# Optimization experiments

Hardware: AMD Instinct MI355X
Metric: run time of the kernel (lower is better)

The kernel has to match this reference:

```python
import jax, jax.numpy as jnp
import numpy as np

NT = 100000   # total word nodes (B graphs * N nodes)
B = 50        # number of graphs in the batch
E = 1600000   # total edges
V = 15000     # vocab (num_word)
D_IN = 128    # h_inp
D_H = 128     # h_dim


def setup_inputs() -> dict:
    key = jax.random.key(0)
    ks = jax.random.split(key, 12)
    return {
        "node_ids": jax.random.randint(ks[0], (NT,), 0, V),
        "src": jax.random.randint(ks[1], (E,), 0, NT),
        "dst": jax.random.randint(ks[2], (E,), 0, NT),
        "edge_weight": jax.random.uniform(ks[3], (E,), dtype=jnp.float32),
        "y_data": jax.random.uniform(ks[4], (B,), dtype=jnp.float32),
        "word_embeds": jax.random.normal(ks[5], (V, D_IN), dtype=jnp.float32) * 0.1,
        "W1": jax.random.normal(ks[6], (D_IN, D_H), dtype=jnp.float32) * 0.05,
        "b1": jax.random.normal(ks[7], (D_H,), dtype=jnp.float32) * 0.05,
        "W2": jax.random.normal(ks[8], (D_H, D_H), dtype=jnp.float32) * 0.05,
        "b2": jax.random.normal(ks[9], (D_H,), dtype=jnp.float32) * 0.05,
        "W_out": jax.random.normal(ks[10], (D_H, 1), dtype=jnp.float32) * 0.05,
        "b_out": jax.random.normal(ks[11], (1,), dtype=jnp.float32) * 0.05,
    }


def _word_graph_layer(h, W, b, src, dst, edge_weight, deg):
    # Linear projection, then DGL u_mul_e + mean aggregation over incoming edges.
    Wh = h @ W + b                                   # [NT, D]
    m = Wh[src] * edge_weight[:, None]               # gather + edge-weight mul, [E, D]
    s = jax.ops.segment_sum(m, dst, num_segments=NT)  # scatter-add, [NT, D]
    # mean over incoming messages; nodes with no in-edges keep 0 (DGL semantics)
    return jnp.where(deg[:, None] > 0, s / jnp.maximum(deg, 1.0)[:, None], 0.0)


def reference(node_ids, src, dst, edge_weight, y_data, word_embeds,
              W1, b1, W2, b2, W_out, b_out):
    deg = jax.ops.segment_sum(jnp.ones_like(edge_weight), dst, num_segments=NT)
    h = word_embeds[node_ids]                        # [NT, D_IN]
    h = _word_graph_layer(h, W1, b1, src, dst, edge_weight, deg)
    h = jax.nn.leaky_relu(h, negative_slope=0.01)
    h = _word_graph_layer(h, W2, b2, src, dst, edge_weight, deg)
    # per-graph mean pool; equal graph sizes so padded mean == true mean
    word_pool = h.reshape(B, NT // B, D_H).mean(axis=1)   # [B, D_H]
    logits = (word_pool @ W_out + b_out).reshape(-1)      # [B]
    # binary_cross_entropy_with_logits, mean reduction (numerically stable)
    loss = jnp.mean(jnp.maximum(logits, 0.0) - logits * y_data
                    + jnp.log1p(jnp.exp(-jnp.abs(logits))))
    y_pred = jax.nn.sigmoid(logits)[:, None]              # [B, 1]
    return (loss, y_pred)
```

## Files before the change

### kernel.cpp

```cpp
#include <hip/hip_runtime.h>
#include <hip/hip_fp16.h>
#include <math.h>

#define NT 100000
#define B_GRAPHS 50
#define NE 1600000
#define V 15000
#define D 128
#define NODES_PER_GRAPH (NT / B_GRAPHS)

#define POOL_N (B_GRAPHS * D + B_GRAPHS)

#define BSH 8
#define BIN_DSTS 256
#define NBIN ((NT + BIN_DSTS - 1) / BIN_DSTS)
#define SLACK (3 * BIN_DSTS)
#define EPB 4096
#define NFB ((NE + EPB - 1) / EPB)
#define BUF_SORT 5632
#define STAGE_STRIDE 4608
#define PAY_STRIDE (STAGE_STRIDE + SLACK)
#define PAY_TAIL 512

__device__ __forceinline__ unsigned enc2_e5m2(float a, float b) {
  unsigned ha = __half_as_ushort(__float2half(a));
  unsigned hb = __half_as_ushort(__float2half(b));
  ha = ((ha + 0x7fu + ((ha >> 8) & 1u)) >> 8) & 0xffu;
  hb = ((hb + 0x7fu + ((hb >> 8) & 1u)) >> 8) & 0xffu;
  return ha | (hb << 8);
}
__device__ __forceinline__ unsigned enc4_e5m2(float a, float b, float c, float d) {
  return enc2_e5m2(a, b) | (enc2_e5m2(c, d) << 16);
}

#define PR 16
__global__ __launch_bounds__(256, 8)
void k_project(const float* __restrict__ embeds,
               const float* __restrict__ W1,
               const float* __restrict__ b1,
               unsigned* __restrict__ P1p8,
               int* __restrict__ binCursor, float* __restrict__ pool,
               int2* __restrict__ payTail) {
  __shared__ float sE[PR][D];
  __shared__ float sO[PR][D];
  int t = threadIdx.x;
  if (blockIdx.x == 0) {
    for (int i = t; i < 512; i += 256) binCursor[i] = 0;
    for (int i = t; i < POOL_N; i += 256) pool[i] = 0.f;
    for (int i = t; i < PAY_TAIL; i += 256) payTail[i] = make_int2(0, 0);
  }
  int row0 = blockIdx.x * PR;
  for (int i = t; i < PR * D; i += 256) {
    int r = i >> 7, c = i & 127;
    int v = row0 + r;
    sE[r][c] = (v < V) ? embeds[(size_t)v * D + c] : 0.f;
  }
  __syncthreads();
  int c = t & 127, rg = (t >> 7) * 8;
  float bd = b1[c];
  float acc[8];
#pragma unroll
  for (int r = 0; r < 8; ++r) acc[r] = bd;
#pragma unroll 4
  for (int k = 0; k < D; ++k) {
    float w = W1[k * D + c];
#pragma unroll
    for (int r = 0; r < 8; ++r) acc[r] = fmaf(sE[rg + r][k], w, acc[r]);
  }
#pragma unroll
  for (int r = 0; r < 8; ++r) sO[rg + r][c] = acc[r];
  __syncthreads();
  for (int i = t; i < PR * 32; i += 256) {
    int r = i >> 5, li = i & 31;
    int v = row0 + r;
    if (v < V)
      P1p8[(size_t)v * 32 + li] =
          enc4_e5m2(sO[r][4 * li], sO[r][4 * li + 1], sO[r][4 * li + 2], sO[r][4 * li + 3]);
  }
}

__global__ __launch_bounds__(512)
void k_binfill(const int* __restrict__ src, const int* __restrict__ dst,
               const float* __restrict__ ew, const int* __restrict__ node_ids,
               int* __restrict__ binCursor, int2* __restrict__ stage) {
  __shared__ int h[512], sc[512], gbase[512], cur[512];
  __shared__ int wsum[8], woff[8];
  __shared__ unsigned short binOf[EPB];
  __shared__ int2 buf[EPB];
  int t = threadIdx.x;
  int lane = t & 63, wv = t >> 6;
  h[t] = 0;
  __syncthreads();
  int base = blockIdx.x * EPB;
  int d_[EPB / 512], b_[EPB / 512];
#pragma unroll
  for (int i = 0; i < EPB / 512; ++i) {
    int e = base + i * 512 + t;
    int d = (e < NE) ? dst[e] : -1;
    d_[i] = d;
    b_[i] = (d >= 0) ? (d >> BSH) : -1;
    if (d >= 0) atomicAdd(&h[b_[i]], 1);
  }
  __syncthreads();
  int c = h[t];
  int v = c;
#pragma unroll
  for (int off = 1; off < 64; off <<= 1) {
    int x = __shfl_up(v, off);
    if (lane >= off) v += x;
  }
  if (lane == 63) wsum[wv] = v;
  __syncthreads();
  if (t == 0) {
    int a = 0;
#pragma unroll
    for (int i = 0; i < 8; ++i) { woff[i] = a; a += wsum[i]; }
  }
  __syncthreads();
  int incl = v + woff[wv];
  sc[t] = incl;
  cur[t] = incl - c;
  if (t < NBIN && c > 0) gbase[t] = atomicAdd(&binCursor[t], c);
  __syncthreads();
  int total = sc[511];
#pragma unroll
  for (int i = 0; i < EPB / 512; ++i) {
    int e = base + i * 512 + t;
    if (e < NE) {
      int s = src[e];
      unsigned uw = __float_as_uint(ew[e]);
      unsigned wb = (uw + 0x7fffu + ((uw >> 16) & 1u)) & 0xffff0000u;
      int wid = node_ids[s];
      int dl = d_[i] & (BIN_DSTS - 1);
      int p = atomicAdd(&cur[b_[i]], 1);
      buf[p] = make_int2((int)(wb | (unsigned)wid), s | (dl << 17));
      binOf[p] = (unsigned short)b_[i];
    }
  }
  __syncthreads();
  for (int i = t; i < total; i += 512) {
    int b = binOf[i];
    int local = i - (sc[b] - h[b]);
    stage[(size_t)b * STAGE_STRIDE + gbase[b] + local] = buf[i];
  }
}

__global__ __launch_bounds__(512)
void k_binsort(const int2* __restrict__ stage, const int* __restrict__ binCnt,
               int* __restrict__ rowD, int* __restrict__ cntD,
               int2* __restrict__ pay) {
  __shared__ int h2[BIN_DSTS], cur2[BIN_DSTS];
  __shared__ float invD[BIN_DSTS];
  __shared__ int wsum4[4], woff4[4];
  __shared__ int sh_end;
  __shared__ int2 buf[BUF_SORT];
  int b = blockIdx.x, t = threadIdx.x;
  int lane = t & 63, wv = t >> 6;
  int cnt = binCnt[b];
  int sb = b * STAGE_STRIDE;
  int pb = b * PAY_STRIDE;
  int dst0 = b << BSH;
  if (t < BIN_DSTS) h2[t] = 0;
  __syncthreads();
  for (int i = t; i < cnt; i += 512)
    atomicAdd(&h2[(stage[sb + i].y >> 17) & 255], 1);
  __syncthreads();
  int c = (t < BIN_DSTS) ? h2[t] : 0;
  int pc = (c + 3) & ~3;
  int v = (t < BIN_DSTS) ? pc : 0;
#pragma unroll
  for (int off = 1; off < 64; off <<= 1) {
    int x = __shfl_up(v, off);
    if (lane >= off) v += x;
  }
  if (lane == 63 && wv < 4) wsum4[wv] = v;
  __syncthreads();
  if (t == 0) {
    int a = 0;
#pragma unroll
    for (int i = 0; i < 4; ++i) { woff4[i] = a; a += wsum4[i]; }
    sh_end = a;
  }
  __syncthreads();
  if (t < BIN_DSTS) {
    int myoff = v + woff4[wv] - pc;
    invD[t] = (c > 0) ? (1.0f / (float)c) : 0.0f;
    cur2[t] = myoff;
    int n = dst0 + t;
    if (n < NT) { rowD[n] = pb + myoff; cntD[n] = c; }
  }
  __syncthreads();
  int end = sh_end + 24;
  if (end > PAY_STRIDE) end = PAY_STRIDE;
  for (int i = t; i < end; i += 512) buf[i] = make_int2(0, 0);
  __syncthreads();
  for (int i = t; i < cnt; i += 512) {
    int2 r = stage[sb + i];
    int dl = (r.y >> 17) & 255;
    float w = __uint_as_float((unsigned)r.x & 0xffff0000u);
    float wp = w * invD[dl];
    unsigned wh = (unsigned)__half_as_ushort(__float2half(wp));
    int p = atomicAdd(&cur2[dl], 1);
    buf[p] = make_int2((int)((wh << 16) | ((unsigned)r.x & 0xffffu)), r.y & 0x1ffff);
  }
  __syncthreads();
  for (int i = t; i < end; i += 512) pay[pb + i] = buf[i];
}

template<bool USE_WID>
__device__ __forceinline__ int pick_idx(const int4& q, int half) {
  int lo = USE_WID ? (q.x & 0xffff) : q.y;
  int hi = USE_WID ? (q.z & 0xffff) : q.w;
  return half ? hi : lo;
}
__device__ __forceinline__ void consume2h(const int4& q, unsigned v, int half,
                                          __half2& A01, __half2& A23, __half2& SW) {
  unsigned wm = (unsigned)(half ? q.z : q.x);
  unsigned wd = (wm >> 16) | (wm & 0xffff0000u);
  unsigned hp0 = ((v & 0xffu) << 8) | ((v & 0xff00u) << 16);
  unsigned hp1 = ((v >> 8) & 0xff00u) | (v & 0xff000000u);
  __half2 w2 = *(__half2*)&wd;
  A01 = __hfma2(w2, *(__half2*)&hp0, A01);
  A23 = __hfma2(w2, *(__half2*)&hp1, A23);
  SW = __hadd2(SW, w2);
}

template<bool USE_WID>
__device__ __forceinline__ void gather_row(const int2* __restrict__ pay,
                                           const unsigned* __restrict__ tab,
                                           int beg, int cnt, int li, int half,
                                           __half2& A01, __half2& A23, __half2& SW) {
  int G = (cnt + 3) >> 2;
  const int4* __restrict__ pp = (const int4*)(pay + beg);
  int4 q0a = pp[0], q0b = pp[1];
  int4 q1a = pp[2], q1b = pp[3];
  int4 q2a = pp[4], q2b = pp[5];
  int4 q3a = pp[6], q3b = pp[7];
  int4 q4a = pp[8], q4b = pp[9];
  unsigned va0 = tab[(size_t)pick_idx<USE_WID>(q0a, half) * 32 + li];
  unsigned vb0 = tab[(size_t)pick_idx<USE_WID>(q0b, half) * 32 + li];
  unsigned va1 = tab[(size_t)pick_idx<USE_WID>(q1a, half) * 32 + li];
  unsigned vb1 = tab[(size_t)pick_idx<USE_WID>(q1b, half) * 32 + li];
  unsigned va2 = tab[(size_t)pick_idx<USE_WID>(q2a, half) * 32 + li];
  unsigned vb2 = tab[(size_t)pick_idx<USE_WID>(q2b, half) * 32 + li];
  for (int g = 0; g < G; ++g) {
    unsigned vn0 = tab[(size_t)pick_idx<USE_WID>(q3a, half) * 32 + li];
    unsigned vn1 = tab[(size_t)pick_idx<USE_WID>(q3b, half) * 32 + li];
    int4 qna = pp[2 * g + 10];
    int4 qnb = pp[2 * g + 11];
    consume2h(q0a, va0, half, A01, A23, SW);
    consume2h(q0b, vb0, half, A01, A23, SW);
    q0a = q1a; q0b = q1b; q1a = q2a; q1b = q2b; q2a = q3a; q2b = q3b;
    q3a = q4a; q3b = q4b; q4a = qna; q4b = qnb;
    va0 = va1; vb0 = vb1; va1 = va2; vb1 = vb2; va2 = vn0; vb2 = vn1;
  }
}

#define NPW1 10
__global__ void k_agg1(const int2* __restrict__ pay,
                       const int* __restrict__ rowD, const int* __restrict__ cntD,
                       const unsigned* __restrict__ P1p8,
                       unsigned* __restrict__ h1p8) {
  int w = threadIdx.x >> 6, lane = threadIdx.x & 63;
  int li = lane & 31, half = lane >> 5;
  int nbase = blockIdx.x * (4 * NPW1) + w * NPW1;
  for (int i = 0; i < NPW1; ++i) {
    int n = nbase + i;
    int beg = __builtin_amdgcn_readfirstlane(rowD[n]);
    int cnt = __builtin_amdgcn_readfirstlane(cntD[n]);
    __half2 A01 = __half2half2(__float2half(0.f));
    __half2 A23 = A01, SW = A01;
    gather_row<true>(pay, P1p8, beg, cnt, li, half, A01, A23, SW);
    float2 f01 = __half22float2(A01);
    float2 f23 = __half22float2(A23);
    float a0 = f01.x, a1 = f01.y, a2 = f23.x, a3 = f23.y;
    a0 += __shfl_down(a0, 32);
    a1 += __shfl_down(a1, 32);
    a2 += __shfl_down(a2, 32);
    a3 += __shfl_down(a3, 32);
    if (lane < 32) {
      float x0 = a0, x1 = a1, x2 = a2, x3 = a3;
      x0 = (x0 > 0.f) ? x0 : 0.01f * x0;
      x1 = (x1 > 0.f) ? x1 : 0.01f * x1;
      x2 = (x2 > 0.f) ? x2 : 0.01f * x2;
      x3 = (x3 > 0.f) ? x3 : 0.01f * x3;
      h1p8[(size_t)n * 32 + li] = enc4_e5m2(x0, x1, x2, x3);
    }
  }
}

#define NPW2 10
#define BLKS_PER_G (NODES_PER_GRAPH / (4 * NPW2))
__global__ void k_agg2(const int2* __restrict__ pay,
                       const int* __restrict__ rowD, const int* __restrict__ cntD,
                       const unsigned* __restrict__ h1p8,
                       float* __restrict__ pool) {
  int g = blockIdx.x / BLKS_PER_G;
  int chunk = blockIdx.x % BLKS_PER_G;
  int w = threadIdx.x >> 6, lane = threadIdx.x & 63;
  int li = lane & 31, half = lane >> 5;
  int nbase = g * NODES_PER_GRAPH + chunk * (4 * NPW2) + w * NPW2;
  __half2 A01 = __half2half2(__float2half(0.f));
  __half2 A23 = A01, SW = A01;
  for (int i = 0; i < NPW2; ++i) {
    int n = nbase + i;
    int beg = __builtin_amdgcn_readfirstlane(rowD[n]);
    int cnt = __builtin_amdgcn_readfirstlane(cntD[n]);
    gather_row<false>(pay, h1p8, beg, cnt, li, half, A01, A23, SW);
  }
  float2 f01 = __half22float2(A01);
  float2 f23 = __half22float2(A23);
  float s0 = f01.x, s1 = f01.y, s2 = f23.x, s3 = f23.y;
  float sc = __low2float(SW);
  s0 += __shfl_down(s0, 32);
  s1 += __shfl_down(s1, 32);
  s2 += __shfl_down(s2, 32);
  s3 += __shfl_down(s3, 32);
  sc += __shfl_down(sc, 32);
  __shared__ float sS[4 * 128];
  __shared__ float sC[4];
  if (lane < 32) {
    sS[w * 128 + 4 * li + 0] = s0;
    sS[w * 128 + 4 * li + 1] = s1;
    sS[w * 128 + 4 * li + 2] = s2;
    sS[w * 128 + 4 * li + 3] = s3;
  }
  if (lane == 0) sC[w] = sc;
  __syncthreads();
  int t = threadIdx.x;
  if (t < 128) {
    float v = sS[t] + sS[128 + t] + sS[256 + t] + sS[384 + t];
    atomicAdd(&pool[g * D + t], v);
  }
  if (t == 0) atomicAdd(&pool[B_GRAPHS * D + g], sC[0] + sC[1] + sC[2] + sC[3]);
}

__global__ void k_final(const float* __restrict__ poolS, const float* __restrict__ poolC,
                        const float* __restrict__ W2, const float* __restrict__ b2,
                        const float* __restrict__ W_out, const float* __restrict__ b_out,
                        const float* __restrict__ y, float* __restrict__ out) {
  __shared__ float w2o[D];
  __shared__ float s2oArr[D];
  __shared__ float s2o_sh;
  __shared__ float logits[64];
  int t = threadIdx.x;
  int w = t >> 6, lane = t & 63;
  if (t < D) {
    float acc = 0.f;
    for (int d = 0; d < D; ++d) acc = fmaf(W2[t * D + d], W_out[d], acc);
    w2o[t] = acc;
  } else {
    int j = t - D;
    s2oArr[j] = b2[j] * W_out[j];
  }
  __syncthreads();
  if (t < 64) {
    float v = s2oArr[lane] + s2oArr[64 + lane];
#pragma unroll
    for (int off = 32; off > 0; off >>= 1) v += __shfl_down(v, off);
    if (lane == 0) s2o_sh = v;
  }
  __syncthreads();
  float s2o = s2o_sh;
  float bout = b_out[0];
  const float invN = 1.0f / (float)NODES_PER_GRAPH;
  for (int g = w; g < B_GRAPHS; g += 4) {
    float v = poolS[g * D + lane] * w2o[lane]
            + poolS[g * D + 64 + lane] * w2o[64 + lane];
#pragma unroll
    for (int off = 32; off > 0; off >>= 1) v += __shfl_down(v, off);
    if (lane == 0) {
      float l = v * invN + poolC[g] * invN * s2o + bout;
      logits[g] = l;
      out[1 + g] = 1.0f / (1.0f + expf(-l));
    }
  }
  __syncthreads();
  if (t < 64) {
    float term = 0.f;
    if (lane < B_GRAPHS) {
      float l = logits[lane];
      term = fmaxf(l, 0.f) - l * y[lane] + log1pf(expf(-fabsf(l)));
    }
#pragma unroll
    for (int off = 32; off > 0; off >>= 1) term += __shfl_down(term, off);
    if (lane == 0) out[0] = term / (float)B_GRAPHS;
  }
}

extern "C" void kernel_launch(void* const* d_in, const int* in_sizes, int n_in,
                              void* d_out, int out_size, void* d_ws, size_t ws_size,
                              hipStream_t stream) {
  const int*   node_ids = (const int*)d_in[0];
  const int*   src      = (const int*)d_in[1];
  const int*   dst      = (const int*)d_in[2];
  const float* ew       = (const float*)d_in[3];
  const float* y        = (const float*)d_in[4];
  const float* embeds   = (const float*)d_in[5];
  const float* W1       = (const float*)d_in[6];
  const float* b1       = (const float*)d_in[7];
  const float* W2       = (const float*)d_in[8];
  const float* b2       = (const float*)d_in[9];
  const float* W_out    = (const float*)d_in[10];
  const float* b_out    = (const float*)d_in[11];
  float* out = (float*)d_out;
  (void)in_sizes; (void)n_in; (void)out_size; (void)ws_size;

  char* ws = (char*)d_ws;
  size_t off = 0;
  auto alloc = [&](size_t bytes) {
    size_t r = off;
    off = (off + bytes + 511) & ~(size_t)511;
    return r;
  };
  size_t o_binCur = alloc(512 * 4);
  size_t o_pool   = alloc((size_t)POOL_N * 4);
  size_t o_rowD   = alloc((size_t)(NT + 1) * 4);
  size_t o_cntD   = alloc((size_t)NT * 4);
  size_t o_P1p8   = alloc((size_t)V * 32 * 4);
  size_t o_h1p8   = alloc((size_t)NT * 32 * 4);
  size_t o_stage  = alloc((size_t)NBIN * STAGE_STRIDE * 8);
  size_t o_pay    = alloc(((size_t)NBIN * PAY_STRIDE + PAY_TAIL) * 8);

  int*      binCursor= (int*)(ws + o_binCur);
  float*    pool     = (float*)(ws + o_pool);
  int*      rowD     = (int*)(ws + o_rowD);
  int*      cntD     = (int*)(ws + o_cntD);
  unsigned* P1p8     = (unsigned*)(ws + o_P1p8);
  unsigned* h1p8     = (unsigned*)(ws + o_h1p8);
  int2*     stage    = (int2*)(ws + o_stage);
  int2*     pay      = (int2*)(ws + o_pay);
  int2*     payTail  = pay + (size_t)NBIN * PAY_STRIDE;

  k_project<<<(V + PR - 1) / PR, 256, 0, stream>>>(embeds, W1, b1, P1p8,
                                                   binCursor, pool, payTail);
  k_binfill<<<NFB, 512, 0, stream>>>(src, dst, ew, node_ids, binCursor, stage);
  k_binsort<<<NBIN, 512, 0, stream>>>(stage, binCursor, rowD, cntD, pay);
  k_agg1<<<NT / (4 * NPW1), 256, 0, stream>>>(pay, rowD, cntD, P1p8, h1p8);
  k_agg2<<<B_GRAPHS * BLKS_PER_G, 256, 0, stream>>>(pay, rowD, cntD, h1p8, pool);
  k_final<<<1, 256, 0, stream>>>(pool, pool + B_GRAPHS * D, W2, b2, W_out, b_out, y, out);
}
```

Measured before the change: 253.7 us.

## Fuse projection with bin-fill and layer-1 aggregation into bin-sort kernel

```diff
diff --git a/kernel.cpp b/kernel.cpp
--- a/kernel.cpp
+++ b/kernel.cpp
@@ -21,6 +21,8 @@
 #define STAGE_STRIDE 4608
 #define PAY_STRIDE (STAGE_STRIDE + SLACK)
 #define PAY_TAIL 512
+#define PR 16
+#define PROJ_BLOCKS ((V + PR - 1) / PR)
 
 __device__ __forceinline__ unsigned enc2_e5m2(float a, float b) {
   unsigned ha = __half_as_ushort(__float2half(a));
@@ -31,180 +33,6 @@
 }
 __device__ __forceinline__ unsigned enc4_e5m2(float a, float b, float c, float d) {
   return enc2_e5m2(a, b) | (enc2_e5m2(c, d) << 16);
-}
-
-#define PR 16
-__global__ __launch_bounds__(256, 8)
-void k_project(const float* __restrict__ embeds,
-               const float* __restrict__ W1,
-               const float* __restrict__ b1,
-               unsigned* __restrict__ P1p8,
-               int* __restrict__ binCursor, float* __restrict__ pool,
-               int2* __restrict__ payTail) {
-  __shared__ float sE[PR][D];
-  __shared__ float sO[PR][D];
-  int t = threadIdx.x;
-  if (blockIdx.x == 0) {
-    for (int i = t; i < 512; i += 256) binCursor[i] = 0;
-    for (int i = t; i < POOL_N; i += 256) pool[i] = 0.f;
-    for (int i = t; i < PAY_TAIL; i += 256) payTail[i] = make_int2(0, 0);
-  }
-  int row0 = blockIdx.x * PR;
-  for (int i = t; i < PR * D; i += 256) {
-    int r = i >> 7, c = i & 127;
-    int v = row0 + r;
-    sE[r][c] = (v < V) ? embeds[(size_t)v * D + c] : 0.f;
-  }
-  __syncthreads();
-  int c = t & 127, rg = (t >> 7) * 8;
-  float bd = b1[c];
-  float acc[8];
-#pragma unroll
-  for (int r = 0; r < 8; ++r) acc[r] = bd;
-#pragma unroll 4
-  for (int k = 0; k < D; ++k) {
-    float w = W1[k * D + c];
-#pragma unroll
-    for (int r = 0; r < 8; ++r) acc[r] = fmaf(sE[rg + r][k], w, acc[r]);
-  }
-#pragma unroll
-  for (int r = 0; r < 8; ++r) sO[rg + r][c] = acc[r];
-  __syncthreads();
-  for (int i = t; i < PR * 32; i += 256) {
-    int r = i >> 5, li = i & 31;
-    int v = row0 + r;
-    if (v < V)
-      P1p8[(size_t)v * 32 + li] =
-          enc4_e5m2(sO[r][4 * li], sO[r][4 * li + 1], sO[r][4 * li + 2], sO[r][4 * li + 3]);
-  }
-}
-
-__global__ __launch_bounds__(512)
-void k_binfill(const int* __restrict__ src, const int* __restrict__ dst,
-               const float* __restrict__ ew, const int* __restrict__ node_ids,
-               int* __restrict__ binCursor, int2* __restrict__ stage) {
-  __shared__ int h[512], sc[512], gbase[512], cur[512];
-  __shared__ int wsum[8], woff[8];
-  __shared__ unsigned short binOf[EPB];
-  __shared__ int2 buf[EPB];
-  int t = threadIdx.x;
-  int lane = t & 63, wv = t >> 6;
-  h[t] = 0;
-  __syncthreads();
-  int base = blockIdx.x * EPB;
-  int d_[EPB / 512], b_[EPB / 512];
-#pragma unroll
-  for (int i = 0; i < EPB / 512; ++i) {
-    int e = base + i * 512 + t;
-    int d = (e < NE) ? dst[e] : -1;
-    d_[i] = d;
-    b_[i] = (d >= 0) ? (d >> BSH) : -1;
-    if (d >= 0) atomicAdd(&h[b_[i]], 1);
-  }
-  __syncthreads();
-  int c = h[t];
-  int v = c;
-#pragma unroll
-  for (int off = 1; off < 64; off <<= 1) {
-    int x = __shfl_up(v, off);
-    if (lane >= off) v += x;
-  }
-  if (lane == 63) wsum[wv] = v;
-  __syncthreads();
-  if (t == 0) {
-    int a = 0;
-#pragma unroll
-    for (int i = 0; i < 8; ++i) { woff[i] = a; a += wsum[i]; }
-  }
-  __syncthreads();
-  int incl = v + woff[wv];
-  sc[t] = incl;
-  cur[t] = incl - c;
-  if (t < NBIN && c > 0) gbase[t] = atomicAdd(&binCursor[t], c);
-  __syncthreads();
-  int total = sc[511];
-#pragma unroll
-  for (int i = 0; i < EPB / 512; ++i) {
-    int e = base + i * 512 + t;
-    if (e < NE) {
-      int s = src[e];
-      unsigned uw = __float_as_uint(ew[e]);
-      unsigned wb = (uw + 0x7fffu + ((uw >> 16) & 1u)) & 0xffff0000u;
-      int wid = node_ids[s];
-      int dl = d_[i] & (BIN_DSTS - 1);
-      int p = atomicAdd(&cur[b_[i]], 1);
-      buf[p] = make_int2((int)(wb | (unsigned)wid), s | (dl << 17));
-      binOf[p] = (unsigned short)b_[i];
-    }
-  }
-  __syncthreads();
-  for (int i = t; i < total; i += 512) {
-    int b = binOf[i];
-    int local = i - (sc[b] - h[b]);
-    stage[(size_t)b * STAGE_STRIDE + gbase[b] + local] = buf[i];
-  }
-}
-
-__global__ __launch_bounds__(512)
-void k_binsort(const int2* __restrict__ stage, const int* __restrict__ binCnt,
-               int* __restrict__ rowD, int* __restrict__ cntD,
-               int2* __restrict__ pay) {
-  __shared__ int h2[BIN_DSTS], cur2[BIN_DSTS];
-  __shared__ float invD[BIN_DSTS];
-  __shared__ int wsum4[4], woff4[4];
-  __shared__ int sh_end;
-  __shared__ int2 buf[BUF_SORT];
-  int b = blockIdx.x, t = threadIdx.x;
-  int lane = t & 63, wv = t >> 6;
-  int cnt = binCnt[b];
-  int sb = b * STAGE_STRIDE;
-  int pb = b * PAY_STRIDE;
-  int dst0 = b << BSH;
-  if (t < BIN_DSTS) h2[t] = 0;
-  __syncthreads();
-  for (int i = t; i < cnt; i += 512)
-    atomicAdd(&h2[(stage[sb + i].y >> 17) & 255], 1);
-  __syncthreads();
-  int c = (t < BIN_DSTS) ? h2[t] : 0;
-  int pc = (c + 3) & ~3;
-  int v = (t < BIN_DSTS) ? pc : 0;
-#pragma unroll
-  for (int off = 1; off < 64; off <<= 1) {
-    int x = __shfl_up(v, off);
-    if (lane >= off) v += x;
-  }
-  if (lane == 63 && wv < 4) wsum4[wv] = v;
-  __syncthreads();
-  if (t == 0) {
-    int a = 0;
-#pragma unroll
-    for (int i = 0; i < 4; ++i) { woff4[i] = a; a += wsum4[i]; }
-    sh_end = a;
-  }
-  __syncthreads();
-  if (t < BIN_DSTS) {
-    int myoff = v + woff4[wv] - pc;
-    invD[t] = (c > 0) ? (1.0f / (float)c) : 0.0f;
-    cur2[t] = myoff;
-    int n = dst0 + t;
-    if (n < NT) { rowD[n] = pb + myoff; cntD[n] = c; }
-  }
-  __syncthreads();
-  int end = sh_end + 24;
-  if (end > PAY_STRIDE) end = PAY_STRIDE;
-  for (int i = t; i < end; i += 512) buf[i] = make_int2(0, 0);
-  __syncthreads();
-  for (int i = t; i < cnt; i += 512) {
-    int2 r = stage[sb + i];
-    int dl = (r.y >> 17) & 255;
-    float w = __uint_as_float((unsigned)r.x & 0xffff0000u);
-    float wp = w * invD[dl];
-    unsigned wh = (unsigned)__half_as_ushort(__float2half(wp));
-    int p = atomicAdd(&cur2[dl], 1);
-    buf[p] = make_int2((int)((wh << 16) | ((unsigned)r.x & 0xffffu)), r.y & 0x1ffff);
-  }
-  __syncthreads();
-  for (int i = t; i < end; i += 512) pay[pb + i] = buf[i];
 }
 
 template<bool USE_WID>
@@ -224,53 +52,221 @@
   A23 = __hfma2(w2, *(__half2*)&hp1, A23);
   SW = __hadd2(SW, w2);
 }
-
-template<bool USE_WID>
-__device__ __forceinline__ void gather_row(const int2* __restrict__ pay,
-                                           const unsigned* __restrict__ tab,
-                                           int beg, int cnt, int li, int half,
-                                           __half2& A01, __half2& A23, __half2& SW) {
-  int G = (cnt + 3) >> 2;
-  const int4* __restrict__ pp = (const int4*)(pay + beg);
-  int4 q0a = pp[0], q0b = pp[1];
-  int4 q1a = pp[2], q1b = pp[3];
-  int4 q2a = pp[4], q2b = pp[5];
-  int4 q3a = pp[6], q3b = pp[7];
-  int4 q4a = pp[8], q4b = pp[9];
-  unsigned va0 = tab[(size_t)pick_idx<USE_WID>(q0a, half) * 32 + li];
-  unsigned vb0 = tab[(size_t)pick_idx<USE_WID>(q0b, half) * 32 + li];
-  unsigned va1 = tab[(size_t)pick_idx<USE_WID>(q1a, half) * 32 + li];
-  unsigned vb1 = tab[(size_t)pick_idx<USE_WID>(q1b, half) * 32 + li];
-  unsigned va2 = tab[(size_t)pick_idx<USE_WID>(q2a, half) * 32 + li];
-  unsigned vb2 = tab[(size_t)pick_idx<USE_WID>(q2b, half) * 32 + li];
-  for (int g = 0; g < G; ++g) {
-    unsigned vn0 = tab[(size_t)pick_idx<USE_WID>(q3a, half) * 32 + li];
-    unsigned vn1 = tab[(size_t)pick_idx<USE_WID>(q3b, half) * 32 + li];
-    int4 qna = pp[2 * g + 10];
-    int4 qnb = pp[2 * g + 11];
-    consume2h(q0a, va0, half, A01, A23, SW);
-    consume2h(q0b, vb0, half, A01, A23, SW);
-    q0a = q1a; q0b = q1b; q1a = q2a; q1b = q2b; q2a = q3a; q2b = q3b;
-    q3a = q4a; q3b = q4b; q4a = qna; q4b = qnb;
-    va0 = va1; vb0 = vb1; va1 = va2; vb1 = vb2; va2 = vn0; vb2 = vn1;
-  }
-}
-
-#define NPW1 10
-__global__ void k_agg1(const int2* __restrict__ pay,
-                       const int* __restrict__ rowD, const int* __restrict__ cntD,
-                       const unsigned* __restrict__ P1p8,
-                       unsigned* __restrict__ h1p8) {
-  int w = threadIdx.x >> 6, lane = threadIdx.x & 63;
+__device__ __forceinline__ void consume2h_ns(const int4& q, unsigned v, int half,
+                                             __half2& A01, __half2& A23) {
+  unsigned wm = (unsigned)(half ? q.z : q.x);
+  unsigned wd = (wm >> 16) | (wm & 0xffff0000u);
+  unsigned hp0 = ((v & 0xffu) << 8) | ((v & 0xff00u) << 16);
+  unsigned hp1 = ((v >> 8) & 0xff00u) | (v & 0xff000000u);
+  __half2 w2 = *(__half2*)&wd;
+  A01 = __hfma2(w2, *(__half2*)&hp0, A01);
+  A23 = __hfma2(w2, *(__half2*)&hp1, A23);
+}
+__device__ __forceinline__ int4 ld2s(const int2* bp, int i) {
+  int2 a = bp[i], c = bp[i + 1];
+  return make_int4(a.x, a.y, c.x, c.y);
+}
+
+__global__ __launch_bounds__(512)
+void k_pb(const float* __restrict__ embeds, const float* __restrict__ W1,
+          const float* __restrict__ b1, unsigned* __restrict__ P1p8,
+          float* __restrict__ pool, int2* __restrict__ payTail,
+          const int* __restrict__ src, const int* __restrict__ dst,
+          const float* __restrict__ ew, const int* __restrict__ node_ids,
+          int* __restrict__ binCursor, int2* __restrict__ stage) {
+  __shared__ union {
+    struct {
+      int h[512], sc[512], gbase[512], cur[512];
+      int wsum[8], woff[8];
+      unsigned short binOf[EPB];
+      int2 buf[EPB];
+    } f;
+    struct {
+      float sE[PR][D];
+      float sO[PR][D];
+    } p;
+  } U;
+  int t = threadIdx.x;
+  if (blockIdx.x < NFB) {
+    int lane = t & 63, wv = t >> 6;
+    U.f.h[t] = 0;
+    __syncthreads();
+    int base = blockIdx.x * EPB;
+    int d_[EPB / 512], b_[EPB / 512];
+#pragma unroll
+    for (int i = 0; i < EPB / 512; ++i) {
+      int e = base + i * 512 + t;
+      int d = (e < NE) ? dst[e] : -1;
+      d_[i] = d;
+      b_[i] = (d >= 0) ? (d >> BSH) : -1;
+      if (d >= 0) atomicAdd(&U.f.h[b_[i]], 1);
+    }
+    __syncthreads();
+    int c = U.f.h[t];
+    int v = c;
+#pragma unroll
+    for (int off = 1; off < 64; off <<= 1) {
+      int x = __shfl_up(v, off);
+      if (lane >= off) v += x;
+    }
+    if (lane == 63) U.f.wsum[wv] = v;
+    __syncthreads();
+    if (t == 0) {
+      int a = 0;
+#pragma unroll
+      for (int i = 0; i < 8; ++i) { U.f.woff[i] = a; a += U.f.wsum[i]; }
+    }
+    __syncthreads();
+    int incl = v + U.f.woff[wv];
+    U.f.sc[t] = incl;
+    U.f.cur[t] = incl - c;
+    if (t < NBIN && c > 0) U.f.gbase[t] = atomicAdd(&binCursor[t], c);
+    __syncthreads();
+    int total = U.f.sc[511];
+#pragma unroll
+    for (int i = 0; i < EPB / 512; ++i) {
+      int e = base + i * 512 + t;
+      if (e < NE) {
+        int s = src[e];
+        unsigned uw = __float_as_uint(ew[e]);
+        unsigned wb = (uw + 0x7fffu + ((uw >> 16) & 1u)) & 0xffff0000u;
+        int wid = node_ids[s];
+        int dl = d_[i] & (BIN_DSTS - 1);
+        int p = atomicAdd(&U.f.cur[b_[i]], 1);
+        U.f.buf[p] = make_int2((int)(wb | (unsigned)wid), s | (dl << 17));
+        U.f.binOf[p] = (unsigned short)b_[i];
+      }
+    }
+    __syncthreads();
+    for (int i = t; i < total; i += 512) {
+      int b = U.f.binOf[i];
+      int local = i - (U.f.sc[b] - U.f.h[b]);
+      stage[(size_t)b * STAGE_STRIDE + U.f.gbase[b] + local] = U.f.buf[i];
+    }
+  } else {
+    int pb = blockIdx.x - NFB;
+    if (pb == 0) {
+      for (int i = t; i < POOL_N; i += 512) pool[i] = 0.f;
+      for (int i = t; i < PAY_TAIL; i += 512) payTail[i] = make_int2(0, 0);
+    }
+    int row0 = pb * PR;
+    for (int i = t; i < PR * D; i += 512) {
+      int r = i >> 7, c = i & 127;
+      int vv = row0 + r;
+      U.p.sE[r][c] = (vv < V) ? embeds[(size_t)vv * D + c] : 0.f;
+    }
+    __syncthreads();
+    int c = t & 127, rg = (t >> 7) * 4;
+    float bd = b1[c];
+    float acc[4];
+#pragma unroll
+    for (int r = 0; r < 4; ++r) acc[r] = bd;
+#pragma unroll 4
+    for (int k = 0; k < D; ++k) {
+      float w = W1[k * D + c];
+#pragma unroll
+      for (int r = 0; r < 4; ++r) acc[r] = fmaf(U.p.sE[rg + r][k], w, acc[r]);
+    }
+#pragma unroll
+    for (int r = 0; r < 4; ++r) U.p.sO[rg + r][c] = acc[r];
+    __syncthreads();
+    {
+      int r = t >> 5, li = t & 31;
+      int vv = row0 + r;
+      if (vv < V)
+        P1p8[(size_t)vv * 32 + li] =
+            enc4_e5m2(U.p.sO[r][4 * li], U.p.sO[r][4 * li + 1],
+                      U.p.sO[r][4 * li + 2], U.p.sO[r][4 * li + 3]);
+    }
+  }
+}
+
+__global__ __launch_bounds__(512)
+void k_sortagg(const int2* __restrict__ stage, const int* __restrict__ binCnt,
+               const unsigned* __restrict__ P1p8,
+               int* __restrict__ rowD, int* __restrict__ cntD,
+               int2* __restrict__ pay, unsigned* __restrict__ h1p8) {
+  __shared__ int h2[BIN_DSTS], cur2[BIN_DSTS], offArr[BIN_DSTS];
+  __shared__ float invD[BIN_DSTS];
+  __shared__ int wsum4[4], woff4[4];
+  __shared__ int sh_end;
+  __shared__ int2 buf[BUF_SORT];
+  int b = blockIdx.x, t = threadIdx.x;
+  int lane = t & 63, wv = t >> 6;
+  int cnt = binCnt[b];
+  int sb = b * STAGE_STRIDE;
+  int pbase = b * PAY_STRIDE;
+  int dst0 = b << BSH;
+  if (t < BIN_DSTS) h2[t] = 0;
+  __syncthreads();
+  for (int i = t; i < cnt; i += 512)
+    atomicAdd(&h2[(stage[sb + i].y >> 17) & 255], 1);
+  __syncthreads();
+  int c = (t < BIN_DSTS) ? h2[t] : 0;
+  int pc = (c + 3) & ~3;
+  int v = (t < BIN_DSTS) ? pc : 0;
+#pragma unroll
+  for (int off = 1; off < 64; off <<= 1) {
+    int x = __shfl_up(v, off);
+    if (lane >= off) v += x;
+  }
+  if (lane == 63 && wv < 4) wsum4[wv] = v;
+  __syncthreads();
+  if (t == 0) {
+    int a = 0;
+#pragma unroll
+    for (int i = 0; i < 4; ++i) { woff4[i] = a; a += wsum4[i]; }
+    sh_end = a;
+  }
+  __syncthreads();
+  if (t < BIN_DSTS) {
+    int myoff = v + woff4[wv] - pc;
+    invD[t] = (c > 0) ? (1.0f / (float)c) : 0.0f;
+    cur2[t] = myoff;
+    offArr[t] = myoff;
+    int n = dst0 + t;
+    if (n < NT) { rowD[n] = pbase + myoff; cntD[n] = c; }
+  }
+  __syncthreads();
+  int end = sh_end + 24;
+  if (end > PAY_STRIDE) end = PAY_STRIDE;
+  for (int i = t; i < end; i += 512) buf[i] = make_int2(0, 0);
+  __syncthreads();
+  for (int i = t; i < cnt; i += 512) {
+    int2 r = stage[sb + i];
+    int dl = (r.y >> 17) & 255;
+    float w = __uint_as_float((unsigned)r.x & 0xffff0000u);
+    float wp = w * invD[dl];
+    unsigned wh = (unsigned)__half_as_ushort(__float2half(wp));
+    int p = atomicAdd(&cur2[dl], 1);
+    buf[p] = make_int2((int)((wh << 16) | ((unsigned)r.x & 0xffffu)), r.y & 0x1ffff);
+  }
+  __syncthreads();
+  for (int i = t; i < end; i += 512) pay[pbase + i] = buf[i];
   int li = lane & 31, half = lane >> 5;
-  int nbase = blockIdx.x * (4 * NPW1) + w * NPW1;
-  for (int i = 0; i < NPW1; ++i) {
-    int n = nbase + i;
-    int beg = __builtin_amdgcn_readfirstlane(rowD[n]);
-    int cnt = __builtin_amdgcn_readfirstlane(cntD[n]);
+  for (int j = 0; j < 32; ++j) {
+    int dl = wv * 32 + j;
+    int beg = offArr[dl];
+    int cn = h2[dl];
+    int G = (cn + 3) >> 2;
     __half2 A01 = __half2half2(__float2half(0.f));
-    __half2 A23 = A01, SW = A01;
-    gather_row<true>(pay, P1p8, beg, cnt, li, half, A01, A23, SW);
+    __half2 A23 = A01;
+    int4 qa0 = ld2s(buf, beg + 0), qb0 = ld2s(buf, beg + 2);
+    int4 qa1 = ld2s(buf, beg + 4), qb1 = ld2s(buf, beg + 6);
+    unsigned va0 = P1p8[(size_t)pick_idx<true>(qa0, half) * 32 + li];
+    unsigned vb0 = P1p8[(size_t)pick_idx<true>(qb0, half) * 32 + li];
+    unsigned va1 = P1p8[(size_t)pick_idx<true>(qa1, half) * 32 + li];
+    unsigned vb1 = P1p8[(size_t)pick_idx<true>(qb1, half) * 32 + li];
+    for (int g = 0; g < G; ++g) {
+      int4 qa2 = ld2s(buf, beg + 4 * g + 8);
+      int4 qb2 = ld2s(buf, beg + 4 * g + 10);
+      unsigned vn0 = P1p8[(size_t)pick_idx<true>(qa2, half) * 32 + li];
+      unsigned vn1 = P1p8[(size_t)pick_idx<true>(qb2, half) * 32 + li];
+      consume2h_ns(qa0, va0, half, A01, A23);
+      consume2h_ns(qb0, vb0, half, A01, A23);
+      qa0 = qa1; qb0 = qb1; qa1 = qa2; qb1 = qb2;
+      va0 = va1; vb0 = vb1; va1 = vn0; vb1 = vn1;
+    }
     float2 f01 = __half22float2(A01);
     float2 f23 = __half22float2(A23);
     float a0 = f01.x, a1 = f01.y, a2 = f23.x, a3 = f23.y;
@@ -279,13 +275,46 @@
     a2 += __shfl_down(a2, 32);
     a3 += __shfl_down(a3, 32);
     if (lane < 32) {
-      float x0 = a0, x1 = a1, x2 = a2, x3 = a3;
-      x0 = (x0 > 0.f) ? x0 : 0.01f * x0;
-      x1 = (x1 > 0.f) ? x1 : 0.01f * x1;
-      x2 = (x2 > 0.f) ? x2 : 0.01f * x2;
-      x3 = (x3 > 0.f) ? x3 : 0.01f * x3;
-      h1p8[(size_t)n * 32 + li] = enc4_e5m2(x0, x1, x2, x3);
-    }
+      int n = dst0 + dl;
+      if (n < NT) {
+        float x0 = a0, x1 = a1, x2 = a2, x3 = a3;
+        x0 = (x0 > 0.f) ? x0 : 0.01f * x0;
+        x1 = (x1 > 0.f) ? x1 : 0.01f * x1;
+        x2 = (x2 > 0.f) ? x2 : 0.01f * x2;
+        x3 = (x3 > 0.f) ? x3 : 0.01f * x3;
+        h1p8[(size_t)n * 32 + li] = enc4_e5m2(x0, x1, x2, x3);
+      }
+    }
+  }
+}
+
+__device__ __forceinline__ void gather_row_g(const int2* __restrict__ pay,
+                                             const unsigned* __restrict__ tab,
+                                             int beg, int cnt, int li, int half,
+                                             __half2& A01, __half2& A23, __half2& SW) {
+  int G = (cnt + 3) >> 2;
+  const int4* __restrict__ pp = (const int4*)(pay + beg);
+  int4 q0a = pp[0], q0b = pp[1];
+  int4 q1a = pp[2], q1b = pp[3];
+  int4 q2a = pp[4], q2b = pp[5];
+  int4 q3a = pp[6], q3b = pp[7];
+  int4 q4a = pp[8], q4b = pp[9];
+  unsigned va0 = tab[(size_t)pick_idx<false>(q0a, half) * 32 + li];
+  unsigned vb0 = tab[(size_t)pick_idx<false>(q0b, half) * 32 + li];
+  unsigned va1 = tab[(size_t)pick_idx<false>(q1a, half) * 32 + li];
+  unsigned vb1 = tab[(size_t)pick_idx<false>(q1b, half) * 32 + li];
+  unsigned va2 = tab[(size_t)pick_idx<false>(q2a, half) * 32 + li];
+  unsigned vb2 = tab[(size_t)pick_idx<false>(q2b, half) * 32 + li];
+  for (int g = 0; g < G; ++g) {
+    unsigned vn0 = tab[(size_t)pick_idx<false>(q3a, half) * 32 + li];
+    unsigned vn1 = tab[(size_t)pick_idx<false>(q3b, half) * 32 + li];
+    int4 qna = pp[2 * g + 10];
+    int4 qnb = pp[2 * g + 11];
+    consume2h(q0a, va0, half, A01, A23, SW);
+    consume2h(q0b, vb0, half, A01, A23, SW);
+    q0a = q1a; q0b = q1b; q1a = q2a; q1b = q2b; q2a = q3a; q2b = q3b;
+    q3a = q4a; q3b = q4b; q4a = qna; q4b = qnb;
+    va0 = va1; vb0 = vb1; va1 = va2; vb1 = vb2; va2 = vn0; vb2 = vn1;
   }
 }
 
@@ -306,7 +335,7 @@
     int n = nbase + i;
     int beg = __builtin_amdgcn_readfirstlane(rowD[n]);
     int cnt = __builtin_amdgcn_readfirstlane(cntD[n]);
-    gather_row<false>(pay, h1p8, beg, cnt, li, half, A01, A23, SW);
+    gather_row_g(pay, h1p8, beg, cnt, li, half, A01, A23, SW);
   }
   float2 f01 = __half22float2(A01);
   float2 f23 = __half22float2(A23);
@@ -432,11 +461,10 @@
   int2*     pay      = (int2*)(ws + o_pay);
   int2*     payTail  = pay + (size_t)NBIN * PAY_STRIDE;
 
-  k_project<<<(V + PR - 1) / PR, 256, 0, stream>>>(embeds, W1, b1, P1p8,
-                                                   binCursor, pool, payTail);
-  k_binfill<<<NFB, 512, 0, stream>>>(src, dst, ew, node_ids, binCursor, stage);
-  k_binsort<<<NBIN, 512, 0, stream>>>(stage, binCursor, rowD, cntD, pay);
-  k_agg1<<<NT / (4 * NPW1), 256, 0, stream>>>(pay, rowD, cntD, P1p8, h1p8);
+  hipMemsetAsync(binCursor, 0, 512 * 4, stream);
+  k_pb<<<NFB + PROJ_BLOCKS, 512, 0, stream>>>(embeds, W1, b1, P1p8, pool, payTail,
+                                              src, dst, ew, node_ids, binCursor, stage);
+  k_sortagg<<<NBIN, 512, 0, stream>>>(stage, binCursor, P1p8, rowD, cntD, pay, h1p8);
   k_agg2<<<B_GRAPHS * BLKS_PER_G, 256, 0, stream>>>(pay, rowD, cntD, h1p8, pool);
   k_final<<<1, 256, 0, stream>>>(pool, pool + B_GRAPHS * D, W2, b2, W_out, b_out, y, out);
 }
```

After: 255.7 us. No clear change (+0.8%).
